# Performance work log

Measured on AMD Instinct MI355X. Metric: run time of the kernel, lower is better.

The kernel has to match this reference:

```python
import jax, jax.numpy as jnp
import numpy as np

C, N, E = 256, 256, 2048          # subgraphs, nodes/subgraph, edges/subgraph
F_IN, NHID, DDI = 128, 128, 256
K1, K2, K3 = 128, 64, 32          # top-k sizes for pooling_ratio=0.5
P, B = 16, 16                     # DAG hierarchy: P parents x B leaf children
GN = C + P + 1                    # global DAG nodes (leaves + parents + root)
GE = 8192                         # global pos/neg edge count


def setup_inputs():
    key = jax.random.key(0)
    ks = jax.random.split(key, 16)
    inp = {
        "x": jax.random.normal(ks[0], (C, N, F_IN), jnp.float32),
        "edge_index": jax.random.randint(ks[1], (C, 2, E), 0, N),
        "edge_weight": jax.random.uniform(ks[2], (C, E), dtype=jnp.float32),
        "global_edge_index": jax.random.randint(ks[3], (2, GE), 0, GN),
        "neg_edge_index": jax.random.randint(ks[4], (2, GE), 0, GN),
    }
    names = [("W1", F_IN, NHID), ("Wp1", NHID, 1), ("W2", NHID, NHID),
             ("Wp2", NHID, 1), ("W3", NHID, NHID), ("Wp3", NHID, 1),
             ("Wg", 6 * NHID, DDI), ("Wl1", DDI, DDI), ("Wl2", DDI, DDI)]
    for i, (nm, fi, fo) in enumerate(names):
        inp[nm] = jax.random.normal(ks[5 + i], (fi, fo), jnp.float32) / np.sqrt(fi)
        inp["b" + nm[1:]] = jnp.zeros((fo,), jnp.float32)
    return inp


def gcn(x, ei, ew, W, b):
    """PyG GCNConv with self-loops: D^-1/2 (A+I) D^-1/2 X W + b."""
    n = x.shape[0]
    h = x @ W
    row, col = ei[0], ei[1]
    deg = 1.0 + jax.ops.segment_sum(ew, col, num_segments=n)
    dis = jax.lax.rsqrt(deg)
    norm = dis[row] * ew * dis[col]                       # [E]
    agg = jax.ops.segment_sum(norm[:, None] * h[row], col, num_segments=n)
    return agg + h / deg[:, None] + b


def sag_pool(x, ei, ew, Ws, bs, k):
    """SAGPooling: GCN score, per-graph top-k, gate by tanh(score), edge filter."""
    n = x.shape[0]
    score = gcn(x, ei, ew, Ws, bs)[:, 0]
    vals, perm = jax.lax.top_k(score, k)
    x_new = x[perm] * jnp.tanh(vals)[:, None]
    newid = jnp.full((n,), -1, jnp.int32).at[perm].set(jnp.arange(k, dtype=jnp.int32))
    r, c = newid[ei[0]], newid[ei[1]]
    keep = (r >= 0) & (c >= 0)
    ei_new = jnp.where(keep, jnp.stack([r, c]), 0)        # dropped edges -> node 0
    ew_new = jnp.where(keep, ew, 0.0)                     # with zero weight
    return x_new, ei_new, ew_new


def _subgraph(x, ei, ew, W1, b1, Wp1, bp1, W2, b2, Wp2, bp2, W3, b3, Wp3, bp3):
    x = jax.nn.relu(gcn(x, ei, ew, W1, b1))
    x, ei, ew = sag_pool(x, ei, ew, Wp1, bp1, K1)
    x1 = jnp.concatenate([x.max(0), x.mean(0)])           # gmp||gap, batch all-zero
    x = jax.nn.relu(gcn(x, ei, ew, W2, b2))
    x, ei, ew = sag_pool(x, ei, ew, Wp2, bp2, K2)
    x2 = jnp.concatenate([x.max(0), x.mean(0)])
    x = jax.nn.relu(gcn(x, ei, ew, W3, b3))
    x, ei, ew = sag_pool(x, ei, ew, Wp3, bp3, K3)
    x3 = jnp.concatenate([x.max(0), x.mean(0)])
    return jnp.concatenate([x1, x2, x3])                  # [6*NHID]


def reference(x, edge_index, edge_weight, global_edge_index, neg_edge_index,
              W1, b1, Wp1, bp1, W2, b2, Wp2, bp2, W3, b3, Wp3, bp3,
              Wg, bg, Wl1, bl1, Wl2, bl2):
    # per-class subgraph pipeline, vmapped over the C subgraphs
    leaf = jax.vmap(_subgraph, in_axes=(0, 0, 0) + (None,) * 12)(
        x, edge_index, edge_weight,
        W1, b1, Wp1, bp1, W2, b2, Wp2, bp2, W3, b3, Wp3, bp3)   # [C, 6*NHID]
    # Get_Fs: mean-aggregate children features up the DAG (fixed 2-level + root)
    parent = leaf.reshape(P, B, -1).mean(axis=1)                # [P, 6*NHID]
    root = parent.mean(axis=0, keepdims=True)                   # [1, 6*NHID]
    gfeat = jnp.concatenate([leaf, parent, root], axis=0)       # [GN, 6*NHID]
    # global GCN (unit edge weights)
    gx = jax.nn.relu(gcn(gfeat, global_edge_index,
                         jnp.ones((GE,), gfeat.dtype), Wg, bg)) # [GN, DDI]
    class_embedding = gx[:C]
    # feature_split + lin1/lin2 + dot-product scores
    pos_s = gx[global_edge_index[0]] @ Wl1 + bl1
    pos_t = gx[global_edge_index[1]] @ Wl2 + bl2
    neg_s = gx[neg_edge_index[0]] @ Wl1 + bl1
    neg_t = gx[neg_edge_index[1]] @ Wl2 + bl2
    pos = jnp.sum(pos_s * pos_t, axis=1)
    neg = jnp.sum(neg_s * neg_t, axis=1)
    # BCEWithLogits: targets 1 for pos, 0 for neg
    loss = jnp.mean(jax.nn.softplus(-pos)) + jnp.mean(jax.nn.softplus(neg))
    return class_embedding, loss
```

## Files before the change

### kernel.cpp

```cpp
#include <hip/hip_runtime.h>
#include <math.h>

#define NT 1024
#define EDGES 2048
#define SENT 0xFFFF

struct SmemA {
  float xbuf[256 * 128];
  unsigned short rc[EDGES];
  float ewl[EDGES];
  unsigned short csr_row[EDGES];
  float csr_coef[EDGES];
  float degs[256];
  float diss[256];
  int   csr_off[257];
  int   csr_cnt[256];
  float hsv[256];
  float scorev[256];
  float vals[128];
  short perm[128];
  signed char newid[256];
};

__device__ __forceinline__ float4* xvec(float* xb, int row, int c4) {
  return reinterpret_cast<float4*>(xb + (row << 7) + ((c4 ^ (row & 7)) << 2));
}
__device__ __forceinline__ int xidx(int row, int col) {
  return (row << 7) + ((((col >> 2) ^ (row & 7)) << 2) | (col & 3));
}

template<int NN, int K, bool FIRST, bool REMAP>
__device__ __forceinline__ void run_stage(
    SmemA& sm,
    const float* __restrict__ xg,
    const int* __restrict__ eic,
    const float* __restrict__ ewc,
    const float* __restrict__ W,
    const float* __restrict__ b,
    const float* __restrict__ Wp,
    const float* __restrict__ bp,
    float* __restrict__ leaf_out,
    float& lmax, float& lmean)
{
  constexpr int NPT  = NN / 64;
  constexpr int Q    = NN / 64;
  constexpr int SEG  = NT / NN;
  constexpr int LEN  = NN / SEG;
  constexpr int LOG  = (NN == 256) ? 8 : (NN == 128 ? 7 : 6);
  const int tid  = threadIdx.x;
  const int lane = tid & 63;
  const int fbase = __builtin_amdgcn_readfirstlane((tid >> 6) << 3);
  const int c4b   = fbase >> 2;

  if (FIRST) {
    if (tid < NN) { sm.degs[tid] = 1.0f; sm.csr_cnt[tid] = 0; }
    __syncthreads();
    const float4* xg4 = reinterpret_cast<const float4*>(xg);
    for (int i = tid; i < 256 * 32; i += NT) {
      const float4 v = xg4[i];
      *xvec(sm.xbuf, i >> 5, i & 31) = v;
    }
    for (int e = tid; e < EDGES; e += NT) {
      const int row = eic[e], col = eic[EDGES + e];
      const float w = ewc[e];
      sm.rc[e]  = (unsigned short)((row << 8) | col);
      sm.ewl[e] = w;
      atomicAdd(&sm.degs[col], w);
      atomicAdd(&sm.csr_cnt[col], 1);
    }
    __syncthreads();
  }

  if (tid < NN) sm.diss[tid] = rsqrtf(sm.degs[tid]);
  if (tid < 64) {
    int c[Q], pre[Q];
    int tot = 0;
#pragma unroll
    for (int i = 0; i < Q; i++) { c[i] = sm.csr_cnt[tid * Q + i]; pre[i] = tot; tot += c[i]; }
    int inc = tot;
#pragma unroll
    for (int d = 1; d < 64; d <<= 1) {
      const int o = __shfl_up(inc, d, 64);
      if (tid >= d) inc += o;
    }
    const int base = inc - tot;
    if (tid == 0) sm.csr_off[0] = 0;
#pragma unroll
    for (int i = 0; i < Q; i++) {
      sm.csr_off[tid * Q + i + 1] = base + pre[i] + c[i];
      sm.csr_cnt[tid * Q + i] = 0;
    }
  }
  __syncthreads();

  for (int e = tid; e < EDGES; e += NT) {
    const unsigned short r = sm.rc[e];
    if (FIRST || r != SENT) {
      const int row = r >> 8, col = r & 255;
      const int p = atomicAdd(&sm.csr_cnt[col], 1);
      const int s = sm.csr_off[col] + p;
      sm.csr_row[s]  = (unsigned short)row;
      sm.csr_coef[s] = sm.diss[row] * sm.ewl[e];
    }
  }
  __syncthreads();

  float acc[NPT][8];
#pragma unroll
  for (int i = 0; i < NPT; i++)
#pragma unroll
    for (int j = 0; j < 8; j++) acc[i][j] = 0.0f;

#pragma unroll 4
  for (int k4 = 0; k4 < 32; k4++) {
    float4 xv[NPT];
#pragma unroll
    for (int i = 0; i < NPT; i++) xv[i] = *xvec(sm.xbuf, lane + (i << 6), k4);
#pragma unroll
    for (int kk = 0; kk < 4; kk++) {
      const float* wr = W + (((k4 << 2) + kk) << 7) + fbase;
      const float4 wa = *reinterpret_cast<const float4*>(wr);
      const float4 wb = *reinterpret_cast<const float4*>(wr + 4);
      const float wv[8] = {wa.x, wa.y, wa.z, wa.w, wb.x, wb.y, wb.z, wb.w};
#pragma unroll
      for (int i = 0; i < NPT; i++) {
        const float xs = (kk == 0) ? xv[i].x : (kk == 1) ? xv[i].y : (kk == 2) ? xv[i].z : xv[i].w;
#pragma unroll
        for (int j = 0; j < 8; j++) acc[i][j] = fmaf(xs, wv[j], acc[i][j]);
      }
    }
  }
  __syncthreads();

#pragma unroll
  for (int i = 0; i < NPT; i++) {
    const int v = lane + (i << 6);
    *xvec(sm.xbuf, v, c4b)     = make_float4(acc[i][0], acc[i][1], acc[i][2], acc[i][3]);
    *xvec(sm.xbuf, v, c4b + 1) = make_float4(acc[i][4], acc[i][5], acc[i][6], acc[i][7]);
  }
  __syncthreads();

  float agg[NPT][8];
#pragma unroll
  for (int i = 0; i < NPT; i++) {
    const int v = lane + (i << 6);
    const int beg = sm.csr_off[v], end = sm.csr_off[v + 1];
#pragma unroll
    for (int j = 0; j < 8; j++) agg[i][j] = 0.0f;
    int r_nxt = 0; float c_nxt = 0.0f;
    if (beg < end) { r_nxt = sm.csr_row[beg]; c_nxt = sm.csr_coef[beg]; }
    for (int s = beg; s < end; ++s) {
      const int r = r_nxt; const float cf = c_nxt;
      if (s + 1 < end) { r_nxt = sm.csr_row[s + 1]; c_nxt = sm.csr_coef[s + 1]; }
      const float4 lo = *xvec(sm.xbuf, r, c4b);
      const float4 hi = *xvec(sm.xbuf, r, c4b + 1);
      agg[i][0] = fmaf(cf, lo.x, agg[i][0]);
      agg[i][1] = fmaf(cf, lo.y, agg[i][1]);
      agg[i][2] = fmaf(cf, lo.z, agg[i][2]);
      agg[i][3] = fmaf(cf, lo.w, agg[i][3]);
      agg[i][4] = fmaf(cf, hi.x, agg[i][4]);
      agg[i][5] = fmaf(cf, hi.y, agg[i][5]);
      agg[i][6] = fmaf(cf, hi.z, agg[i][6]);
      agg[i][7] = fmaf(cf, hi.w, agg[i][7]);
    }
  }
  if (tid < NN) sm.hsv[tid] = 0.0f;
  __syncthreads();

  {
    const float4 ba = *reinterpret_cast<const float4*>(b + fbase);
    const float4 bb = *reinterpret_cast<const float4*>(b + fbase + 4);
    const float bv[8] = {ba.x, ba.y, ba.z, ba.w, bb.x, bb.y, bb.z, bb.w};
#pragma unroll
    for (int i = 0; i < NPT; i++) {
      const int v = lane + (i << 6);
      const float dv = sm.diss[v];
      const float invd = 1.0f / sm.degs[v];
#pragma unroll
      for (int j = 0; j < 8; j++)
        acc[i][j] = fmaxf(fmaf(agg[i][j], dv, fmaf(acc[i][j], invd, bv[j])), 0.0f);
      *xvec(sm.xbuf, v, c4b)     = make_float4(acc[i][0], acc[i][1], acc[i][2], acc[i][3]);
      *xvec(sm.xbuf, v, c4b + 1) = make_float4(acc[i][4], acc[i][5], acc[i][6], acc[i][7]);
    }
    const float4 wa = *reinterpret_cast<const float4*>(Wp + fbase);
    const float4 wb = *reinterpret_cast<const float4*>(Wp + fbase + 4);
    const float wv[8] = {wa.x, wa.y, wa.z, wa.w, wb.x, wb.y, wb.z, wb.w};
#pragma unroll
    for (int i = 0; i < NPT; i++) {
      float part = 0.0f;
#pragma unroll
      for (int j = 0; j < 8; j++) part = fmaf(acc[i][j], wv[j], part);
      atomicAdd(&sm.hsv[lane + (i << 6)], part);
    }
  }
  __syncthreads();

  if (tid < NN) {
    const int v = tid;
    const int beg = sm.csr_off[v], end = sm.csr_off[v + 1];
    float s = 0.0f;
    for (int e2 = beg; e2 < end; e2++)
      s = fmaf(sm.csr_coef[e2], sm.hsv[sm.csr_row[e2]], s);
    sm.scorev[v] = s * sm.diss[v] + sm.hsv[v] / sm.degs[v] + bp[0];
    sm.csr_cnt[v] = 0;
  }
  __syncthreads();

  {
    const int node = tid & (NN - 1);
    const int seg  = tid >> LOG;
    const float sv = sm.scorev[node];
    int part = 0;
    const int u0 = seg * LEN;
#pragma unroll 4
    for (int u = u0; u < u0 + LEN; u++) {
      const float su = sm.scorev[u];
      part += (su > sv) || (su == sv && u < node);
    }
    if (part) atomicAdd(&sm.csr_cnt[node], part);
  }
  __syncthreads();
  if (tid < NN) {
    const int rank = sm.csr_cnt[tid];
    if (rank < K) { sm.perm[rank] = (short)tid; sm.vals[rank] = sm.scorev[tid]; sm.newid[tid] = (signed char)rank; }
    else sm.newid[tid] = -1;
    if (tid < K) { sm.degs[tid] = 1.0f; sm.csr_cnt[tid] = 0; }
  }
  __syncthreads();

  {
    constexpr int TPR = NT / K;
    constexpr int C4  = 32 / TPR;
    const int drow = tid / TPR;
    const int cc   = (tid % TPR) * C4;
    const int src  = sm.perm[drow];
    const float g  = tanhf(sm.vals[drow]);
    float4 tmp[C4];
#pragma unroll
    for (int j = 0; j < C4; j++) tmp[j] = *xvec(sm.xbuf, src, cc + j);
    __syncthreads();
#pragma unroll
    for (int j = 0; j < C4; j++) {
      tmp[j].x *= g; tmp[j].y *= g; tmp[j].z *= g; tmp[j].w *= g;
      *xvec(sm.xbuf, drow, cc + j) = tmp[j];
    }
  }
  __syncthreads();

  if (tid < 128) {
    float mx = -INFINITY, sv = 0.0f;
    for (int i = 0; i < K; i++) {
      const float v = sm.xbuf[xidx(i, tid)];
      mx = fmaxf(mx, v); sv += v;
    }
    lmax = mx;
    lmean = sv * (1.0f / K);
    leaf_out[tid] = mx;
    leaf_out[128 + tid] = lmean;
  }
  if (REMAP) {
    for (int e = tid; e < EDGES; e += NT) {
      const unsigned short r = sm.rc[e];
      if (FIRST || r != SENT) {
        const int r2 = sm.newid[r >> 8];
        const int c2 = sm.newid[r & 255];
        if (r2 < 0 || c2 < 0) sm.rc[e] = SENT;
        else {
          sm.rc[e] = (unsigned short)((r2 << 8) | c2);
          atomicAdd(&sm.degs[c2], sm.ewl[e]);
          atomicAdd(&sm.csr_cnt[c2], 1);
        }
      }
    }
  }
  __syncthreads();
}

__global__ __launch_bounds__(NT)
void stageA_kernel(const float* __restrict__ x0,
                   const int* __restrict__ ei, const float* __restrict__ ew,
                   const float* __restrict__ W1, const float* __restrict__ b1,
                   const float* __restrict__ Wp1, const float* __restrict__ bp1,
                   const float* __restrict__ W2, const float* __restrict__ b2,
                   const float* __restrict__ Wp2, const float* __restrict__ bp2,
                   const float* __restrict__ W3, const float* __restrict__ b3,
                   const float* __restrict__ Wp3, const float* __restrict__ bp3,
                   const float* __restrict__ Wg,
                   float* __restrict__ gfeat, float* __restrict__ hG)
{
  __shared__ SmemA sm;
  const int c = blockIdx.x;
  const int tid = threadIdx.x;
  if (c == 0 && tid < 256) hG[(size_t)272 * 256 + tid] = 0.0f;
  const int* eic = ei + (size_t)c * 2 * EDGES;
  const float* ewc = ew + (size_t)c * EDGES;
  const float* xgc = x0 + (size_t)c * 256 * 128;
  float* leaf = gfeat + (size_t)c * 768;
  float l0 = 0.f, l1 = 0.f, l2 = 0.f, l3 = 0.f, l4 = 0.f, l5 = 0.f;
  run_stage<256, 128, true,  true >(sm, xgc, eic, ewc, W1, b1, Wp1, bp1, leaf + 0,   l0, l1);
  run_stage<128,  64, false, true >(sm, nullptr, nullptr, nullptr, W2, b2, Wp2, bp2, leaf + 256, l2, l3);
  run_stage< 64,  32, false, false>(sm, nullptr, nullptr, nullptr, W3, b3, Wp3, bp3, leaf + 512, l4, l5);

  float* leafbuf = sm.csr_coef;
  float* hGacc   = sm.degs;
  if (tid < 256) {
    if (tid < 128) {
      leafbuf[tid]       = l0; leafbuf[128 + tid] = l1;
      leafbuf[256 + tid] = l2; leafbuf[384 + tid] = l3;
      leafbuf[512 + tid] = l4; leafbuf[640 + tid] = l5;
    }
    hGacc[tid] = 0.0f;
  }
  __syncthreads();
  {
    const int f = tid & 255, q = tid >> 8;
    const float* wgq = Wg + (size_t)(q * 192) * 256 + f;
    const float* lb  = leafbuf + q * 192;
    float p0 = 0.f, p1 = 0.f, p2 = 0.f, p3 = 0.f;
    for (int i = 0; i < 192; i += 4) {
      p0 = fmaf(lb[i],     wgq[(size_t)i * 256],      p0);
      p1 = fmaf(lb[i + 1], wgq[(size_t)(i + 1) * 256], p1);
      p2 = fmaf(lb[i + 2], wgq[(size_t)(i + 2) * 256], p2);
      p3 = fmaf(lb[i + 3], wgq[(size_t)(i + 3) * 256], p3);
    }
    atomicAdd(&hGacc[f], (p0 + p1) + (p2 + p3));
  }
  __syncthreads();
  if (tid < 256) hG[(size_t)c * 256 + tid] = hGacc[tid];
}

__global__ __launch_bounds__(NT)
void prep_k(const float* __restrict__ gfeat, const float* __restrict__ Wg,
            float* __restrict__ hG, const int* __restrict__ gei,
            float* __restrict__ degG, float* __restrict__ lacc,
            int* __restrict__ lctr) {
  const int tid = threadIdx.x;
  if (blockIdx.x == 16) {
    __shared__ int cnt[273];
    for (int i = tid; i < 273; i += NT) cnt[i] = 0;
    __syncthreads();
    for (int e = tid; e < 8192; e += NT) atomicAdd(&cnt[gei[8192 + e]], 1);
    __syncthreads();
    for (int i = tid; i < 273; i += NT) degG[i] = 1.0f + (float)cnt[i];
    if (tid == 0) { *lacc = 0.0f; *lctr = 0; }
    return;
  }
  const int p = blockIdx.x;
  __shared__ float prow[768];
  __shared__ float hGacc[256];
  for (int k = tid; k < 768; k += NT) {
    float s0 = 0.f, s1 = 0.f;
#pragma unroll
    for (int b2 = 0; b2 < 16; b2 += 2) {
      s0 += gfeat[(size_t)(p * 16 + b2) * 768 + k];
      s1 += gfeat[(size_t)(p * 16 + b2 + 1) * 768 + k];
    }
    prow[k] = (s0 + s1) * (1.0f / 16.0f);
  }
  if (tid < 256) hGacc[tid] = 0.0f;
  __syncthreads();
  {
    const int f = tid & 255, q = tid >> 8;
    const float* wgq = Wg + (size_t)(q * 192) * 256 + f;
    const float* lb  = prow + q * 192;
    float p0 = 0.f, p1 = 0.f, p2 = 0.f, p3 = 0.f;
    for (int i = 0; i < 192; i += 4) {
      p0 = fmaf(lb[i],     wgq[(size_t)i * 256],      p0);
      p1 = fmaf(lb[i + 1], wgq[(size_t)(i + 1) * 256], p1);
      p2 = fmaf(lb[i + 2], wgq[(size_t)(i + 2) * 256], p2);
      p3 = fmaf(lb[i + 3], wgq[(size_t)(i + 3) * 256], p3);
    }
    atomicAdd(&hGacc[f], (p0 + p1) + (p2 + p3));
  }
  __syncthreads();
  if (tid < 256) {
    const float hv = hGacc[tid];
    hG[(size_t)(256 + p) * 256 + tid] = hv;
    atomicAdd(&hG[(size_t)272 * 256 + tid], hv * (1.0f / 16.0f));
  }
}

__global__ __launch_bounds__(256)
void gaggemb_k(const float* __restrict__ hG, const float* __restrict__ degG,
               const int* __restrict__ gei, const float* __restrict__ bg,
               const float* __restrict__ Wl1, const float* __restrict__ bl1,
               const float* __restrict__ Wl2, const float* __restrict__ bl2,
               float* __restrict__ out_ce, float* __restrict__ A,
               float* __restrict__ B) {
  __shared__ int   lrows[512];
  __shared__ float lcoef[512];
  __shared__ float gxr[256];
  __shared__ int   lcnt;
  const int v = blockIdx.x, tid = threadIdx.x;
  if (tid == 0) lcnt = 0;
  __syncthreads();
  for (int e = tid; e < 8192; e += 256)
    if (gei[8192 + e] == v) {
      const int p = atomicAdd(&lcnt, 1);
      if (p < 512) lrows[p] = gei[e];
    }
  __syncthreads();
  const int n = min(lcnt, 512);
  for (int i = tid; i < n; i += 256) lcoef[i] = rsqrtf(degG[lrows[i]]);
  __syncthreads();
  float a0 = 0.f, a1 = 0.f, a2 = 0.f, a3 = 0.f;
  int i = 0;
  for (; i + 4 <= n; i += 4) {
    a0 = fmaf(lcoef[i],     hG[(size_t)lrows[i]     * 256 + tid], a0);
    a1 = fmaf(lcoef[i + 1], hG[(size_t)lrows[i + 1] * 256 + tid], a1);
    a2 = fmaf(lcoef[i + 2], hG[(size_t)lrows[i + 2] * 256 + tid], a2);
    a3 = fmaf(lcoef[i + 3], hG[(size_t)lrows[i + 3] * 256 + tid], a3);
  }
  for (; i < n; i++) a0 = fmaf(lcoef[i], hG[(size_t)lrows[i] * 256 + tid], a0);
  const float dg = degG[v];
  float val = ((a0 + a1) + (a2 + a3)) * rsqrtf(dg)
            + hG[(size_t)v * 256 + tid] / dg + bg[tid];
  val = fmaxf(val, 0.0f);
  gxr[tid] = val;
  if (v < 256) out_ce[(size_t)v * 256 + tid] = val;
  __syncthreads();
  float aa0 = bl1[tid], aa1 = 0.f, aa2 = 0.f, aa3 = 0.f;
  float bb0 = bl2[tid], bb1 = 0.f, bb2 = 0.f, bb3 = 0.f;
  for (int k = 0; k < 256; k += 4) {
    const float g0 = gxr[k], g1 = gxr[k + 1], g2 = gxr[k + 2], g3 = gxr[k + 3];
    aa0 = fmaf(g0, Wl1[(size_t)k * 256 + tid],       aa0);
    aa1 = fmaf(g1, Wl1[(size_t)(k + 1) * 256 + tid], aa1);
    aa2 = fmaf(g2, Wl1[(size_t)(k + 2) * 256 + tid], aa2);
    aa3 = fmaf(g3, Wl1[(size_t)(k + 3) * 256 + tid], aa3);
    bb0 = fmaf(g0, Wl2[(size_t)k * 256 + tid],       bb0);
    bb1 = fmaf(g1, Wl2[(size_t)(k + 1) * 256 + tid], bb1);
    bb2 = fmaf(g2, Wl2[(size_t)(k + 2) * 256 + tid], bb2);
    bb3 = fmaf(g3, Wl2[(size_t)(k + 3) * 256 + tid], bb3);
  }
  A[(size_t)v * 256 + tid] = (aa0 + aa1) + (aa2 + aa3);
  B[(size_t)v * 256 + tid] = (bb0 + bb1) + (bb2 + bb3);
}

__global__ __launch_bounds__(256)
void loss_k(const float* __restrict__ A, const float* __restrict__ B,
            const int* __restrict__ gei, const int* __restrict__ nei,
            float* __restrict__ acc, int* __restrict__ lctr,
            float* __restrict__ out) {
  const int gw = (blockIdx.x * blockDim.x + threadIdx.x) >> 6;
  const int lane = threadIdx.x & 63;
  float lsum = 0.0f;
  for (int idx = gw; idx < 16384; idx += 512) {
    const bool ispos = idx < 8192;
    const int e = ispos ? idx : idx - 8192;
    const int* ia = ispos ? gei : nei;
    const int s = ia[e], t = ia[8192 + e];
    float p = 0.0f;
#pragma unroll
    for (int j = 0; j < 4; j++)
      p += A[(size_t)s * 256 + lane + 64 * j] * B[(size_t)t * 256 + lane + 64 * j];
#pragma unroll
    for (int off = 32; off; off >>= 1) p += __shfl_xor(p, off, 64);
    const float z = ispos ? -p : p;
    lsum += fmaxf(z, 0.0f) + log1pf(expf(-fabsf(z)));
  }
  if (lane == 0) atomicAdd(acc, lsum);
  __syncthreads();
  if (threadIdx.x == 0) {
    __threadfence();
    const int old = atomicAdd(lctr, 1);
    if (old == (int)gridDim.x - 1) {
      const float tot = atomicAdd(acc, 0.0f);
      out[65536] = tot * (1.0f / 8192.0f);
    }
  }
}

extern "C" void kernel_launch(void* const* d_in, const int* in_sizes, int n_in,
                              void* d_out, int out_size, void* d_ws, size_t ws_size,
                              hipStream_t stream) {
  const float* x   = (const float*)d_in[0];
  const int*   ei  = (const int*)d_in[1];
  const float* ew  = (const float*)d_in[2];
  const int*   gei = (const int*)d_in[3];
  const int*   nei = (const int*)d_in[4];
  const float* W1  = (const float*)d_in[5];
  const float* b1  = (const float*)d_in[6];
  const float* Wp1 = (const float*)d_in[7];
  const float* bp1 = (const float*)d_in[8];
  const float* W2  = (const float*)d_in[9];
  const float* b2  = (const float*)d_in[10];
  const float* Wp2 = (const float*)d_in[11];
  const float* bp2 = (const float*)d_in[12];
  const float* W3  = (const float*)d_in[13];
  const float* b3  = (const float*)d_in[14];
  const float* Wp3 = (const float*)d_in[15];
  const float* bp3 = (const float*)d_in[16];
  const float* Wg  = (const float*)d_in[17];
  const float* bg  = (const float*)d_in[18];
  const float* Wl1 = (const float*)d_in[19];
  const float* bl1 = (const float*)d_in[20];
  const float* Wl2 = (const float*)d_in[21];
  const float* bl2 = (const float*)d_in[22];

  float* ws    = (float*)d_ws;
  float* gfeat = ws;
  float* hG    = gfeat + 256 * 768;
  float* degG  = hG + 273 * 256;
  float* Aemb  = degG + 288;
  float* Bemb  = Aemb + 273 * 256;
  float* lacc  = Bemb + 273 * 256;
  int*   lctr  = (int*)(lacc + 1);
  float* out   = (float*)d_out;

  stageA_kernel<<<256, NT, 0, stream>>>(x, ei, ew, W1, b1, Wp1, bp1,
                                        W2, b2, Wp2, bp2, W3, b3, Wp3, bp3,
                                        Wg, gfeat, hG);
  prep_k<<<17, NT, 0, stream>>>(gfeat, Wg, hG, gei, degG, lacc, lctr);
  gaggemb_k<<<273, 256, 0, stream>>>(hG, degG, gei, bg, Wl1, bl1, Wl2, bl2,
                                     out, Aemb, Bemb);
  loss_k<<<128, 256, 0, stream>>>(Aemb, Bemb, gei, nei, lacc, lctr, out);
}
```

Baseline: 182.5 us.

## Fuse all stages into one cooperative kernel and widen per-thread feature tiles

Replaces the four separate kernel launches with a single cooperative mega-kernel that uses grid-wide syncs between the subgraph stage, parent/root aggregation, global GCN plus embedding, and the loss. Each wave now computes 16 features over half the rows instead of 8 features over all rows, changing register tiling in the GEMM and aggregation loops. The root mean is computed from leaf hG directly instead of via atomics from parents. It removes launch gaps and tail effects but relies on all 256 blocks being co-resident, and the extra register pressure could hurt the main stage.

```diff
diff --git a/kernel.cpp b/kernel.cpp
--- a/kernel.cpp
+++ b/kernel.cpp
@@ -1,9 +1,12 @@
 #include <hip/hip_runtime.h>
+#include <hip/hip_cooperative_groups.h>
 #include <math.h>
 
 #define NT 1024
 #define EDGES 2048
 #define SENT 0xFFFF
+
+namespace cg = cooperative_groups;
 
 struct SmemA {
   float xbuf[256 * 128];
@@ -42,15 +45,20 @@
     float* __restrict__ leaf_out,
     float& lmax, float& lmean)
 {
-  constexpr int NPT  = NN / 64;
   constexpr int Q    = NN / 64;
   constexpr int SEG  = NT / NN;
   constexpr int LEN  = NN / SEG;
   constexpr int LOG  = (NN == 256) ? 8 : (NN == 128 ? 7 : 6);
+  constexpr int NPT  = (NN == 256) ? 2 : 1;
   const int tid  = threadIdx.x;
   const int lane = tid & 63;
-  const int fbase = __builtin_amdgcn_readfirstlane((tid >> 6) << 3);
+  const int wid  = tid >> 6;
+  const int fbase = __builtin_amdgcn_readfirstlane((wid & 7) << 4);
   const int c4b   = fbase >> 2;
+  const int rg    = wid >> 3;
+  const int rbase = rg * (NN / 2);
+  const bool act  = (NN > 64) || (lane < 32);
+  const int lrow  = (NN == 64) ? (lane & 31) : lane;
 
   if (FIRST) {
     if (tid < NN) { sm.degs[tid] = 1.0f; sm.csr_cnt[tid] = 0; }
@@ -105,63 +113,72 @@
   }
   __syncthreads();
 
-  float acc[NPT][8];
+  float acc[NPT][16];
 #pragma unroll
   for (int i = 0; i < NPT; i++)
 #pragma unroll
-    for (int j = 0; j < 8; j++) acc[i][j] = 0.0f;
-
-#pragma unroll 4
+    for (int j = 0; j < 16; j++) acc[i][j] = 0.0f;
+
+#pragma unroll 2
   for (int k4 = 0; k4 < 32; k4++) {
     float4 xv[NPT];
 #pragma unroll
-    for (int i = 0; i < NPT; i++) xv[i] = *xvec(sm.xbuf, lane + (i << 6), k4);
+    for (int i = 0; i < NPT; i++) xv[i] = *xvec(sm.xbuf, rbase + lrow + (i << 6), k4);
 #pragma unroll
     for (int kk = 0; kk < 4; kk++) {
       const float* wr = W + (((k4 << 2) + kk) << 7) + fbase;
       const float4 wa = *reinterpret_cast<const float4*>(wr);
       const float4 wb = *reinterpret_cast<const float4*>(wr + 4);
-      const float wv[8] = {wa.x, wa.y, wa.z, wa.w, wb.x, wb.y, wb.z, wb.w};
+      const float4 wc = *reinterpret_cast<const float4*>(wr + 8);
+      const float4 wd = *reinterpret_cast<const float4*>(wr + 12);
+      const float wv[16] = {wa.x, wa.y, wa.z, wa.w, wb.x, wb.y, wb.z, wb.w,
+                            wc.x, wc.y, wc.z, wc.w, wd.x, wd.y, wd.z, wd.w};
 #pragma unroll
       for (int i = 0; i < NPT; i++) {
         const float xs = (kk == 0) ? xv[i].x : (kk == 1) ? xv[i].y : (kk == 2) ? xv[i].z : xv[i].w;
 #pragma unroll
-        for (int j = 0; j < 8; j++) acc[i][j] = fmaf(xs, wv[j], acc[i][j]);
-      }
-    }
-  }
-  __syncthreads();
-
+        for (int j = 0; j < 16; j++) acc[i][j] = fmaf(xs, wv[j], acc[i][j]);
+      }
+    }
+  }
+  __syncthreads();
+
+  if (act) {
+#pragma unroll
+    for (int i = 0; i < NPT; i++) {
+      const int v = rbase + lrow + (i << 6);
+      *xvec(sm.xbuf, v, c4b)     = make_float4(acc[i][0],  acc[i][1],  acc[i][2],  acc[i][3]);
+      *xvec(sm.xbuf, v, c4b + 1) = make_float4(acc[i][4],  acc[i][5],  acc[i][6],  acc[i][7]);
+      *xvec(sm.xbuf, v, c4b + 2) = make_float4(acc[i][8],  acc[i][9],  acc[i][10], acc[i][11]);
+      *xvec(sm.xbuf, v, c4b + 3) = make_float4(acc[i][12], acc[i][13], acc[i][14], acc[i][15]);
+    }
+  }
+  __syncthreads();
+
+  float agg[NPT][16];
 #pragma unroll
   for (int i = 0; i < NPT; i++) {
-    const int v = lane + (i << 6);
-    *xvec(sm.xbuf, v, c4b)     = make_float4(acc[i][0], acc[i][1], acc[i][2], acc[i][3]);
-    *xvec(sm.xbuf, v, c4b + 1) = make_float4(acc[i][4], acc[i][5], acc[i][6], acc[i][7]);
-  }
-  __syncthreads();
-
-  float agg[NPT][8];
-#pragma unroll
-  for (int i = 0; i < NPT; i++) {
-    const int v = lane + (i << 6);
+    const int v = rbase + lrow + (i << 6);
     const int beg = sm.csr_off[v], end = sm.csr_off[v + 1];
 #pragma unroll
-    for (int j = 0; j < 8; j++) agg[i][j] = 0.0f;
+    for (int j = 0; j < 16; j++) agg[i][j] = 0.0f;
     int r_nxt = 0; float c_nxt = 0.0f;
     if (beg < end) { r_nxt = sm.csr_row[beg]; c_nxt = sm.csr_coef[beg]; }
     for (int s = beg; s < end; ++s) {
       const int r = r_nxt; const float cf = c_nxt;
       if (s + 1 < end) { r_nxt = sm.csr_row[s + 1]; c_nxt = sm.csr_coef[s + 1]; }
-      const float4 lo = *xvec(sm.xbuf, r, c4b);
-      const float4 hi = *xvec(sm.xbuf, r, c4b + 1);
-      agg[i][0] = fmaf(cf, lo.x, agg[i][0]);
-      agg[i][1] = fmaf(cf, lo.y, agg[i][1]);
-      agg[i][2] = fmaf(cf, lo.z, agg[i][2]);
-      agg[i][3] = fmaf(cf, lo.w, agg[i][3]);
-      agg[i][4] = fmaf(cf, hi.x, agg[i][4]);
-      agg[i][5] = fmaf(cf, hi.y, agg[i][5]);
-      agg[i][6] = fmaf(cf, hi.z, agg[i][6]);
-      agg[i][7] = fmaf(cf, hi.w, agg[i][7]);
+      const float4 q0 = *xvec(sm.xbuf, r, c4b);
+      const float4 q1 = *xvec(sm.xbuf, r, c4b + 1);
+      const float4 q2 = *xvec(sm.xbuf, r, c4b + 2);
+      const float4 q3 = *xvec(sm.xbuf, r, c4b + 3);
+      agg[i][0]  = fmaf(cf, q0.x, agg[i][0]);  agg[i][1]  = fmaf(cf, q0.y, agg[i][1]);
+      agg[i][2]  = fmaf(cf, q0.z, agg[i][2]);  agg[i][3]  = fmaf(cf, q0.w, agg[i][3]);
+      agg[i][4]  = fmaf(cf, q1.x, agg[i][4]);  agg[i][5]  = fmaf(cf, q1.y, agg[i][5]);
+      agg[i][6]  = fmaf(cf, q1.z, agg[i][6]);  agg[i][7]  = fmaf(cf, q1.w, agg[i][7]);
+      agg[i][8]  = fmaf(cf, q2.x, agg[i][8]);  agg[i][9]  = fmaf(cf, q2.y, agg[i][9]);
+      agg[i][10] = fmaf(cf, q2.z, agg[i][10]); agg[i][11] = fmaf(cf, q2.w, agg[i][11]);
+      agg[i][12] = fmaf(cf, q3.x, agg[i][12]); agg[i][13] = fmaf(cf, q3.y, agg[i][13]);
+      agg[i][14] = fmaf(cf, q3.z, agg[i][14]); agg[i][15] = fmaf(cf, q3.w, agg[i][15]);
     }
   }
   if (tid < NN) sm.hsv[tid] = 0.0f;
@@ -170,27 +187,37 @@
   {
     const float4 ba = *reinterpret_cast<const float4*>(b + fbase);
     const float4 bb = *reinterpret_cast<const float4*>(b + fbase + 4);
-    const float bv[8] = {ba.x, ba.y, ba.z, ba.w, bb.x, bb.y, bb.z, bb.w};
+    const float4 bc = *reinterpret_cast<const float4*>(b + fbase + 8);
+    const float4 bd = *reinterpret_cast<const float4*>(b + fbase + 12);
+    const float bv[16] = {ba.x, ba.y, ba.z, ba.w, bb.x, bb.y, bb.z, bb.w,
+                          bc.x, bc.y, bc.z, bc.w, bd.x, bd.y, bd.z, bd.w};
 #pragma unroll
     for (int i = 0; i < NPT; i++) {
-      const int v = lane + (i << 6);
+      const int v = rbase + lrow + (i << 6);
       const float dv = sm.diss[v];
       const float invd = 1.0f / sm.degs[v];
 #pragma unroll
-      for (int j = 0; j < 8; j++)
+      for (int j = 0; j < 16; j++)
         acc[i][j] = fmaxf(fmaf(agg[i][j], dv, fmaf(acc[i][j], invd, bv[j])), 0.0f);
-      *xvec(sm.xbuf, v, c4b)     = make_float4(acc[i][0], acc[i][1], acc[i][2], acc[i][3]);
-      *xvec(sm.xbuf, v, c4b + 1) = make_float4(acc[i][4], acc[i][5], acc[i][6], acc[i][7]);
+      if (act) {
+        *xvec(sm.xbuf, v, c4b)     = make_float4(acc[i][0],  acc[i][1],  acc[i][2],  acc[i][3]);
+        *xvec(sm.xbuf, v, c4b + 1) = make_float4(acc[i][4],  acc[i][5],  acc[i][6],  acc[i][7]);
+        *xvec(sm.xbuf, v, c4b + 2) = make_float4(acc[i][8],  acc[i][9],  acc[i][10], acc[i][11]);
+        *xvec(sm.xbuf, v, c4b + 3) = make_float4(acc[i][12], acc[i][13], acc[i][14], acc[i][15]);
+      }
     }
     const float4 wa = *reinterpret_cast<const float4*>(Wp + fbase);
     const float4 wb = *reinterpret_cast<const float4*>(Wp + fbase + 4);
-    const float wv[8] = {wa.x, wa.y, wa.z, wa.w, wb.x, wb.y, wb.z, wb.w};
+    const float4 wc = *reinterpret_cast<const float4*>(Wp + fbase + 8);
+    const float4 wd = *reinterpret_cast<const float4*>(Wp + fbase + 12);
+    const float wv[16] = {wa.x, wa.y, wa.z, wa.w, wb.x, wb.y, wb.z, wb.w,
+                          wc.x, wc.y, wc.z, wc.w, wd.x, wd.y, wd.z, wd.w};
 #pragma unroll
     for (int i = 0; i < NPT; i++) {
       float part = 0.0f;
 #pragma unroll
-      for (int j = 0; j < 8; j++) part = fmaf(acc[i][j], wv[j], part);
-      atomicAdd(&sm.hsv[lane + (i << 6)], part);
+      for (int j = 0; j < 16; j++) part = fmaf(acc[i][j], wv[j], part);
+      if (act) atomicAdd(&sm.hsv[rbase + lrow + (i << 6)], part);
     }
   }
   __syncthreads();
@@ -276,196 +303,205 @@
   __syncthreads();
 }
 
-__global__ __launch_bounds__(NT)
-void stageA_kernel(const float* __restrict__ x0,
-                   const int* __restrict__ ei, const float* __restrict__ ew,
-                   const float* __restrict__ W1, const float* __restrict__ b1,
-                   const float* __restrict__ Wp1, const float* __restrict__ bp1,
-                   const float* __restrict__ W2, const float* __restrict__ b2,
-                   const float* __restrict__ Wp2, const float* __restrict__ bp2,
-                   const float* __restrict__ W3, const float* __restrict__ b3,
-                   const float* __restrict__ Wp3, const float* __restrict__ bp3,
-                   const float* __restrict__ Wg,
-                   float* __restrict__ gfeat, float* __restrict__ hG)
+__global__ __launch_bounds__(NT, 1)
+void mega_k(const float* __restrict__ x0,
+            const int* __restrict__ ei, const float* __restrict__ ew,
+            const int* __restrict__ gei, const int* __restrict__ nei,
+            const float* __restrict__ W1, const float* __restrict__ b1,
+            const float* __restrict__ Wp1, const float* __restrict__ bp1,
+            const float* __restrict__ W2, const float* __restrict__ b2,
+            const float* __restrict__ Wp2, const float* __restrict__ bp2,
+            const float* __restrict__ W3, const float* __restrict__ b3,
+            const float* __restrict__ Wp3, const float* __restrict__ bp3,
+            const float* __restrict__ Wg, const float* __restrict__ bg,
+            const float* __restrict__ Wl1, const float* __restrict__ bl1,
+            const float* __restrict__ Wl2, const float* __restrict__ bl2,
+            float* __restrict__ gfeat, float* __restrict__ hG,
+            float* __restrict__ degG, float* __restrict__ A, float* __restrict__ B,
+            float* __restrict__ lacc, int* __restrict__ lctr, float* __restrict__ out)
 {
   __shared__ SmemA sm;
+  cg::grid_group grid = cg::this_grid();
   const int c = blockIdx.x;
   const int tid = threadIdx.x;
-  if (c == 0 && tid < 256) hG[(size_t)272 * 256 + tid] = 0.0f;
-  const int* eic = ei + (size_t)c * 2 * EDGES;
-  const float* ewc = ew + (size_t)c * EDGES;
-  const float* xgc = x0 + (size_t)c * 256 * 128;
-  float* leaf = gfeat + (size_t)c * 768;
-  float l0 = 0.f, l1 = 0.f, l2 = 0.f, l3 = 0.f, l4 = 0.f, l5 = 0.f;
-  run_stage<256, 128, true,  true >(sm, xgc, eic, ewc, W1, b1, Wp1, bp1, leaf + 0,   l0, l1);
-  run_stage<128,  64, false, true >(sm, nullptr, nullptr, nullptr, W2, b2, Wp2, bp2, leaf + 256, l2, l3);
-  run_stage< 64,  32, false, false>(sm, nullptr, nullptr, nullptr, W3, b3, Wp3, bp3, leaf + 512, l4, l5);
-
-  float* leafbuf = sm.csr_coef;
-  float* hGacc   = sm.degs;
-  if (tid < 256) {
-    if (tid < 128) {
-      leafbuf[tid]       = l0; leafbuf[128 + tid] = l1;
-      leafbuf[256 + tid] = l2; leafbuf[384 + tid] = l3;
-      leafbuf[512 + tid] = l4; leafbuf[640 + tid] = l5;
-    }
-    hGacc[tid] = 0.0f;
-  }
-  __syncthreads();
+
   {
-    const int f = tid & 255, q = tid >> 8;
-    const float* wgq = Wg + (size_t)(q * 192) * 256 + f;
-    const float* lb  = leafbuf + q * 192;
-    float p0 = 0.f, p1 = 0.f, p2 = 0.f, p3 = 0.f;
-    for (int i = 0; i < 192; i += 4) {
-      p0 = fmaf(lb[i],     wgq[(size_t)i * 256],      p0);
-      p1 = fmaf(lb[i + 1], wgq[(size_t)(i + 1) * 256], p1);
-      p2 = fmaf(lb[i + 2], wgq[(size_t)(i + 2) * 256], p2);
-      p3 = fmaf(lb[i + 3], wgq[(size_t)(i + 3) * 256], p3);
-    }
-    atomicAdd(&hGacc[f], (p0 + p1) + (p2 + p3));
-  }
-  __syncthreads();
-  if (tid < 256) hG[(size_t)c * 256 + tid] = hGacc[tid];
-}
-
-__global__ __launch_bounds__(NT)
-void prep_k(const float* __restrict__ gfeat, const float* __restrict__ Wg,
-            float* __restrict__ hG, const int* __restrict__ gei,
-            float* __restrict__ degG, float* __restrict__ lacc,
-            int* __restrict__ lctr) {
-  const int tid = threadIdx.x;
-  if (blockIdx.x == 16) {
-    __shared__ int cnt[273];
+    const int* eic = ei + (size_t)c * 2 * EDGES;
+    const float* ewc = ew + (size_t)c * EDGES;
+    const float* xgc = x0 + (size_t)c * 256 * 128;
+    float* leaf = gfeat + (size_t)c * 768;
+    float l0 = 0.f, l1 = 0.f, l2 = 0.f, l3 = 0.f, l4 = 0.f, l5 = 0.f;
+    run_stage<256, 128, true,  true >(sm, xgc, eic, ewc, W1, b1, Wp1, bp1, leaf + 0,   l0, l1);
+    run_stage<128,  64, false, true >(sm, nullptr, nullptr, nullptr, W2, b2, Wp2, bp2, leaf + 256, l2, l3);
+    run_stage< 64,  32, false, false>(sm, nullptr, nullptr, nullptr, W3, b3, Wp3, bp3, leaf + 512, l4, l5);
+
+    float* leafbuf = sm.csr_coef;
+    float* hGacc   = sm.degs;
+    if (tid < 256) {
+      if (tid < 128) {
+        leafbuf[tid]       = l0; leafbuf[128 + tid] = l1;
+        leafbuf[256 + tid] = l2; leafbuf[384 + tid] = l3;
+        leafbuf[512 + tid] = l4; leafbuf[640 + tid] = l5;
+      }
+      hGacc[tid] = 0.0f;
+    }
+    __syncthreads();
+    {
+      const int f = tid & 255, q = tid >> 8;
+      const float* wgq = Wg + (size_t)(q * 192) * 256 + f;
+      const float* lb  = leafbuf + q * 192;
+      float p0 = 0.f, p1 = 0.f, p2 = 0.f, p3 = 0.f;
+      for (int i = 0; i < 192; i += 4) {
+        p0 = fmaf(lb[i],     wgq[(size_t)i * 256],       p0);
+        p1 = fmaf(lb[i + 1], wgq[(size_t)(i + 1) * 256], p1);
+        p2 = fmaf(lb[i + 2], wgq[(size_t)(i + 2) * 256], p2);
+        p3 = fmaf(lb[i + 3], wgq[(size_t)(i + 3) * 256], p3);
+      }
+      atomicAdd(&hGacc[f], (p0 + p1) + (p2 + p3));
+    }
+    __syncthreads();
+    if (tid < 256) hG[(size_t)c * 256 + tid] = hGacc[tid];
+  }
+  grid.sync();
+
+  float* base = sm.xbuf;
+  if (c < 16) {
+    float* prow  = base;
+    float* hGacc = base + 768;
+    for (int k = tid; k < 768; k += NT) {
+      float s0 = 0.f, s1 = 0.f;
+#pragma unroll
+      for (int b2 = 0; b2 < 16; b2 += 2) {
+        s0 += gfeat[(size_t)(c * 16 + b2) * 768 + k];
+        s1 += gfeat[(size_t)(c * 16 + b2 + 1) * 768 + k];
+      }
+      prow[k] = (s0 + s1) * (1.0f / 16.0f);
+    }
+    if (tid < 256) hGacc[tid] = 0.0f;
+    __syncthreads();
+    {
+      const int f = tid & 255, q = tid >> 8;
+      const float* wgq = Wg + (size_t)(q * 192) * 256 + f;
+      const float* lb  = prow + q * 192;
+      float p0 = 0.f, p1 = 0.f, p2 = 0.f, p3 = 0.f;
+      for (int i = 0; i < 192; i += 4) {
+        p0 = fmaf(lb[i],     wgq[(size_t)i * 256],       p0);
+        p1 = fmaf(lb[i + 1], wgq[(size_t)(i + 1) * 256], p1);
+        p2 = fmaf(lb[i + 2], wgq[(size_t)(i + 2) * 256], p2);
+        p3 = fmaf(lb[i + 3], wgq[(size_t)(i + 3) * 256], p3);
+      }
+      atomicAdd(&hGacc[f], (p0 + p1) + (p2 + p3));
+    }
+    __syncthreads();
+    if (tid < 256) hG[(size_t)(256 + c) * 256 + tid] = hGacc[tid];
+  } else if (c == 16) {
+    int* cnt = (int*)base;
     for (int i = tid; i < 273; i += NT) cnt[i] = 0;
     __syncthreads();
     for (int e = tid; e < 8192; e += NT) atomicAdd(&cnt[gei[8192 + e]], 1);
     __syncthreads();
     for (int i = tid; i < 273; i += NT) degG[i] = 1.0f + (float)cnt[i];
     if (tid == 0) { *lacc = 0.0f; *lctr = 0; }
-    return;
-  }
-  const int p = blockIdx.x;
-  __shared__ float prow[768];
-  __shared__ float hGacc[256];
-  for (int k = tid; k < 768; k += NT) {
-    float s0 = 0.f, s1 = 0.f;
-#pragma unroll
-    for (int b2 = 0; b2 < 16; b2 += 2) {
-      s0 += gfeat[(size_t)(p * 16 + b2) * 768 + k];
-      s1 += gfeat[(size_t)(p * 16 + b2 + 1) * 768 + k];
-    }
-    prow[k] = (s0 + s1) * (1.0f / 16.0f);
-  }
-  if (tid < 256) hGacc[tid] = 0.0f;
-  __syncthreads();
+  } else if (c == 17) {
+    float* acc4 = base;
+    const int f = tid & 255, q = tid >> 8;
+    float s = 0.f;
+    for (int r = q; r < 256; r += 4) s += hG[(size_t)r * 256 + f];
+    acc4[(q << 8) + f] = s;
+    __syncthreads();
+    if (tid < 256)
+      hG[(size_t)272 * 256 + tid] =
+        (acc4[tid] + acc4[256 + tid] + acc4[512 + tid] + acc4[768 + tid]) * (1.0f / 256.0f);
+  }
+  grid.sync();
+
   {
-    const int f = tid & 255, q = tid >> 8;
-    const float* wgq = Wg + (size_t)(q * 192) * 256 + f;
-    const float* lb  = prow + q * 192;
-    float p0 = 0.f, p1 = 0.f, p2 = 0.f, p3 = 0.f;
-    for (int i = 0; i < 192; i += 4) {
-      p0 = fmaf(lb[i],     wgq[(size_t)i * 256],      p0);
-      p1 = fmaf(lb[i + 1], wgq[(size_t)(i + 1) * 256], p1);
-      p2 = fmaf(lb[i + 2], wgq[(size_t)(i + 2) * 256], p2);
-      p3 = fmaf(lb[i + 3], wgq[(size_t)(i + 3) * 256], p3);
-    }
-    atomicAdd(&hGacc[f], (p0 + p1) + (p2 + p3));
-  }
-  __syncthreads();
-  if (tid < 256) {
-    const float hv = hGacc[tid];
-    hG[(size_t)(256 + p) * 256 + tid] = hv;
-    atomicAdd(&hG[(size_t)272 * 256 + tid], hv * (1.0f / 16.0f));
-  }
-}
-
-__global__ __launch_bounds__(256)
-void gaggemb_k(const float* __restrict__ hG, const float* __restrict__ degG,
-               const int* __restrict__ gei, const float* __restrict__ bg,
-               const float* __restrict__ Wl1, const float* __restrict__ bl1,
-               const float* __restrict__ Wl2, const float* __restrict__ bl2,
-               float* __restrict__ out_ce, float* __restrict__ A,
-               float* __restrict__ B) {
-  __shared__ int   lrows[512];
-  __shared__ float lcoef[512];
-  __shared__ float gxr[256];
-  __shared__ int   lcnt;
-  const int v = blockIdx.x, tid = threadIdx.x;
-  if (tid == 0) lcnt = 0;
-  __syncthreads();
-  for (int e = tid; e < 8192; e += 256)
-    if (gei[8192 + e] == v) {
-      const int p = atomicAdd(&lcnt, 1);
-      if (p < 512) lrows[p] = gei[e];
-    }
-  __syncthreads();
-  const int n = min(lcnt, 512);
-  for (int i = tid; i < n; i += 256) lcoef[i] = rsqrtf(degG[lrows[i]]);
-  __syncthreads();
-  float a0 = 0.f, a1 = 0.f, a2 = 0.f, a3 = 0.f;
-  int i = 0;
-  for (; i + 4 <= n; i += 4) {
-    a0 = fmaf(lcoef[i],     hG[(size_t)lrows[i]     * 256 + tid], a0);
-    a1 = fmaf(lcoef[i + 1], hG[(size_t)lrows[i + 1] * 256 + tid], a1);
-    a2 = fmaf(lcoef[i + 2], hG[(size_t)lrows[i + 2] * 256 + tid], a2);
-    a3 = fmaf(lcoef[i + 3], hG[(size_t)lrows[i + 3] * 256 + tid], a3);
-  }
-  for (; i < n; i++) a0 = fmaf(lcoef[i], hG[(size_t)lrows[i] * 256 + tid], a0);
-  const float dg = degG[v];
-  float val = ((a0 + a1) + (a2 + a3)) * rsqrtf(dg)
-            + hG[(size_t)v * 256 + tid] / dg + bg[tid];
-  val = fmaxf(val, 0.0f);
-  gxr[tid] = val;
-  if (v < 256) out_ce[(size_t)v * 256 + tid] = val;
-  __syncthreads();
-  float aa0 = bl1[tid], aa1 = 0.f, aa2 = 0.f, aa3 = 0.f;
-  float bb0 = bl2[tid], bb1 = 0.f, bb2 = 0.f, bb3 = 0.f;
-  for (int k = 0; k < 256; k += 4) {
-    const float g0 = gxr[k], g1 = gxr[k + 1], g2 = gxr[k + 2], g3 = gxr[k + 3];
-    aa0 = fmaf(g0, Wl1[(size_t)k * 256 + tid],       aa0);
-    aa1 = fmaf(g1, Wl1[(size_t)(k + 1) * 256 + tid], aa1);
-    aa2 = fmaf(g2, Wl1[(size_t)(k + 2) * 256 + tid], aa2);
-    aa3 = fmaf(g3, Wl1[(size_t)(k + 3) * 256 + tid], aa3);
-    bb0 = fmaf(g0, Wl2[(size_t)k * 256 + tid],       bb0);
-    bb1 = fmaf(g1, Wl2[(size_t)(k + 1) * 256 + tid], bb1);
-    bb2 = fmaf(g2, Wl2[(size_t)(k + 2) * 256 + tid], bb2);
-    bb3 = fmaf(g3, Wl2[(size_t)(k + 3) * 256 + tid], bb3);
-  }
-  A[(size_t)v * 256 + tid] = (aa0 + aa1) + (aa2 + aa3);
-  B[(size_t)v * 256 + tid] = (bb0 + bb1) + (bb2 + bb3);
-}
-
-__global__ __launch_bounds__(256)
-void loss_k(const float* __restrict__ A, const float* __restrict__ B,
-            const int* __restrict__ gei, const int* __restrict__ nei,
-            float* __restrict__ acc, int* __restrict__ lctr,
-            float* __restrict__ out) {
-  const int gw = (blockIdx.x * blockDim.x + threadIdx.x) >> 6;
-  const int lane = threadIdx.x & 63;
-  float lsum = 0.0f;
-  for (int idx = gw; idx < 16384; idx += 512) {
-    const bool ispos = idx < 8192;
-    const int e = ispos ? idx : idx - 8192;
-    const int* ia = ispos ? gei : nei;
-    const int s = ia[e], t = ia[8192 + e];
-    float p = 0.0f;
-#pragma unroll
-    for (int j = 0; j < 4; j++)
-      p += A[(size_t)s * 256 + lane + 64 * j] * B[(size_t)t * 256 + lane + 64 * j];
-#pragma unroll
-    for (int off = 32; off; off >>= 1) p += __shfl_xor(p, off, 64);
-    const float z = ispos ? -p : p;
-    lsum += fmaxf(z, 0.0f) + log1pf(expf(-fabsf(z)));
-  }
-  if (lane == 0) atomicAdd(acc, lsum);
-  __syncthreads();
-  if (threadIdx.x == 0) {
-    __threadfence();
-    const int old = atomicAdd(lctr, 1);
-    if (old == (int)gridDim.x - 1) {
-      const float tot = atomicAdd(acc, 0.0f);
-      out[65536] = tot * (1.0f / 8192.0f);
+    int*   lrows = (int*)base;
+    float* lcoef = base + 512;
+    float* gxr   = base + 1024;
+    float* pacc  = base + 1280;
+    float* pacc2 = base + 2304;
+    int*   lcnt  = (int*)(base + 3328);
+    for (int rr = 0; rr < 2; rr++) {
+      if (rr == 1 && c >= 17) break;
+      const int v = rr ? 256 + c : c;
+      if (tid == 0) *lcnt = 0;
+      __syncthreads();
+      for (int e = tid; e < 8192; e += NT)
+        if (gei[8192 + e] == v) { int p = atomicAdd(lcnt, 1); if (p < 512) lrows[p] = gei[e]; }
+      __syncthreads();
+      const int n = min(*lcnt, 512);
+      for (int i = tid; i < n; i += NT) lcoef[i] = rsqrtf(degG[lrows[i]]);
+      __syncthreads();
+      {
+        const int f = tid & 255, q = tid >> 8;
+        float s = 0.f;
+        for (int i = q; i < n; i += 4) s = fmaf(lcoef[i], hG[(size_t)lrows[i] * 256 + f], s);
+        pacc[(q << 8) + f] = s;
+      }
+      __syncthreads();
+      if (tid < 256) {
+        const float dg = degG[v];
+        float val = (pacc[tid] + pacc[256 + tid] + pacc[512 + tid] + pacc[768 + tid]) * rsqrtf(dg)
+                  + hG[(size_t)v * 256 + tid] / dg + bg[tid];
+        val = fmaxf(val, 0.0f);
+        gxr[tid] = val;
+        if (v < 256) out[(size_t)v * 256 + tid] = val;
+      }
+      __syncthreads();
+      {
+        const int f = tid & 255, q = tid >> 8;
+        const int k0 = q << 6;
+        float a = 0.f, b2 = 0.f;
+        for (int k = k0; k < k0 + 64; k++) {
+          const float g = gxr[k];
+          a  = fmaf(g, Wl1[(size_t)k * 256 + f], a);
+          b2 = fmaf(g, Wl2[(size_t)k * 256 + f], b2);
+        }
+        pacc[(q << 8) + f] = a; pacc2[(q << 8) + f] = b2;
+      }
+      __syncthreads();
+      if (tid < 256) {
+        A[(size_t)v * 256 + tid] = pacc[tid] + pacc[256 + tid] + pacc[512 + tid] + pacc[768 + tid] + bl1[tid];
+        B[(size_t)v * 256 + tid] = pacc2[tid] + pacc2[256 + tid] + pacc2[512 + tid] + pacc2[768 + tid] + bl2[tid];
+      }
+      __syncthreads();
+    }
+  }
+  grid.sync();
+
+  {
+    if (tid == 0) base[0] = 0.0f;
+    __syncthreads();
+    const int gw16 = (c << 4) + (tid >> 6);
+    const int lane = tid & 63;
+    float lsum = 0.0f;
+#pragma unroll
+    for (int j = 0; j < 4; j++) {
+      const int idx = (gw16 << 2) + j;
+      const bool ispos = idx < 8192;
+      const int e = idx & 8191;
+      const int* ia = ispos ? gei : nei;
+      const int s2 = ia[e], t2 = ia[8192 + e];
+      float p = 0.0f;
+#pragma unroll
+      for (int m = 0; m < 4; m++)
+        p += A[(size_t)s2 * 256 + lane + (m << 6)] * B[(size_t)t2 * 256 + lane + (m << 6)];
+#pragma unroll
+      for (int off = 32; off; off >>= 1) p += __shfl_xor(p, off, 64);
+      const float z = ispos ? -p : p;
+      lsum += fmaxf(z, 0.0f) + log1pf(expf(-fabsf(z)));
+    }
+    if (lane == 0) atomicAdd(&base[0], lsum);
+    __syncthreads();
+    if (tid == 0) {
+      atomicAdd(lacc, base[0]);
+      __threadfence();
+      const int old = atomicAdd(lctr, 1);
+      if (old == 255) {
+        const float tot = atomicAdd(lacc, 0.0f);
+        out[65536] = tot * (1.0f / 8192.0f);
+      }
     }
   }
 }
@@ -507,11 +543,14 @@
   int*   lctr  = (int*)(lacc + 1);
   float* out   = (float*)d_out;
 
-  stageA_kernel<<<256, NT, 0, stream>>>(x, ei, ew, W1, b1, Wp1, bp1,
-                                        W2, b2, Wp2, bp2, W3, b3, Wp3, bp3,
-                                        Wg, gfeat, hG);
-  prep_k<<<17, NT, 0, stream>>>(gfeat, Wg, hG, gei, degG, lacc, lctr);
-  gaggemb_k<<<273, 256, 0, stream>>>(hG, degG, gei, bg, Wl1, bl1, Wl2, bl2,
-                                     out, Aemb, Bemb);
-  loss_k<<<128, 256, 0, stream>>>(Aemb, Bemb, gei, nei, lacc, lctr, out);
+  void* args[] = {
+    (void*)&x, (void*)&ei, (void*)&ew, (void*)&gei, (void*)&nei,
+    (void*)&W1, (void*)&b1, (void*)&Wp1, (void*)&bp1,
+    (void*)&W2, (void*)&b2, (void*)&Wp2, (void*)&bp2,
+    (void*)&W3, (void*)&b3, (void*)&Wp3, (void*)&bp3,
+    (void*)&Wg, (void*)&bg, (void*)&Wl1, (void*)&bl1, (void*)&Wl2, (void*)&bl2,
+    (void*)&gfeat, (void*)&hG, (void*)&degG, (void*)&Aemb, (void*)&Bemb,
+    (void*)&lacc, (void*)&lctr, (void*)&out
+  };
+  hipLaunchCooperativeKernel((const void*)mega_k, dim3(256), dim3(NT), args, 0, stream);
 }
```

Measured after the change: 343.0 us. 88.0% more time.
